# Kernel tuning notes

Hardware: AMD Instinct MI355X
Metric: run time of the kernel (lower is better)

The kernel has to match this reference:

```python
import math
import jax, jax.numpy as jnp
import numpy as np

Q = 24
N = 8
T_THETA = 1.0
R_S = 3.0
SIGMA_R = 1.0
RHO_MIN = 0.05
N_ORI = 4
TOL = 0.5


def _build_bank_7x7(n, tol=0.5, eps=1e-06):
    m = 3
    coords = np.arange(-m, m + 1, dtype=np.float32)
    u = coords.reshape(1, 1, 7)  # varies along width
    v = coords.reshape(1, 7, 1)  # varies along height
    Delta = math.pi / float(n)
    thetas = ((0.5 * Delta + np.arange(n, dtype=np.float32) * Delta) % math.pi).reshape(n, 1, 1)
    d = np.abs(-np.sin(thetas) * u + np.cos(thetas) * v)
    M = (d <= tol).astype(np.float32)
    M[:, m, m] = 1.0
    W = M[:, None, :, :]  # (n,1,7,7)
    denom = W.sum(axis=(1, 2, 3), keepdims=True) + eps
    return W / denom


def _bilinear_shift(Fm, dx, dy):
    """Shift-sample Fm (B,H,W) by (dx,dy) pixels, matching torch grid_sample
    (bilinear, zeros padding, align_corners=False) on linspace(-1,1) base grid."""
    B, H, W = Fm.shape
    xs = (jnp.arange(W, dtype=Fm.dtype) - dx) * (W / (W - 1)) - 0.5
    ys = (jnp.arange(H, dtype=Fm.dtype) - dy) * (H / (H - 1)) - 0.5

    def axis_parts(p, size):
        p0 = jnp.floor(p)
        f = p - p0
        i0 = p0.astype(jnp.int32)
        i1 = i0 + 1
        w0 = jnp.where((i0 >= 0) & (i0 < size), 1.0 - f, 0.0)
        w1 = jnp.where((i1 >= 0) & (i1 < size), f, 0.0)
        return jnp.clip(i0, 0, size - 1), jnp.clip(i1, 0, size - 1), w0, w1

    y0, y1, wy0, wy1 = axis_parts(ys, H)
    x0, x1, wx0, wx1 = axis_parts(xs, W)
    # separable bilinear: interpolate rows, then columns
    Fy = Fm[:, y0, :] * wy0[None, :, None] + Fm[:, y1, :] * wy1[None, :, None]
    return Fy[:, :, x0] * wx0[None, None, :] + Fy[:, :, x1] * wx1[None, None, :]


def _line_energy_theta(x):
    """x: (B,2,H,W) -> hat_theta (B,H,W) in [0, 2pi)."""
    Fm = jnp.sqrt(jnp.sum(x * x, axis=1))  # (B,H,W) L2 over channels
    t_n = jnp.arange(1, N + 1, dtype=x.dtype) / N * R_S
    w_n = jnp.exp(-t_n * t_n / (2.0 * SIGMA_R ** 2))
    w_n = w_n / w_n.sum()
    theta_q = 2.0 * jnp.pi * jnp.arange(Q, dtype=x.dtype) / Q
    cos_q, sin_q = jnp.cos(theta_q), jnp.sin(theta_q)

    def energy_one_angle(cs):
        c, s = cs
        # (N,B,H,W) samples along the ray, then radial weighted sum
        S = jax.vmap(lambda t: _bilinear_shift(Fm, t * c, t * s))(t_n)
        return jnp.tensordot(w_n, S, axes=1)  # (B,H,W)

    E = jax.lax.map(energy_one_angle, (cos_q, sin_q))  # (Q,B,H,W)
    pi_q = jax.nn.softmax(E / T_THETA, axis=0)
    sy = jnp.einsum('q,qbhw->bhw', sin_q, pi_q)
    cx = jnp.einsum('q,qbhw->bhw', cos_q, pi_q)
    hat = jnp.arctan2(sy, cx)
    return jnp.remainder(hat + 2.0 * jnp.pi, 2.0 * jnp.pi)


def setup_inputs() -> dict:
    key = jax.random.key(0)
    k1, = jax.random.split(key, 1)
    x = jax.random.normal(k1, (8, 2, 512, 512), dtype=jnp.float32)
    gain = jnp.ones((1,), dtype=jnp.float32)
    log_route_temp = jnp.asarray(math.log(0.08), dtype=jnp.float32)
    rho_scaled = (0.5 - RHO_MIN) / (1.0 - RHO_MIN)
    rho_logit = jnp.asarray(math.log(rho_scaled / (1.0 - rho_scaled)), dtype=jnp.float32)
    W_bank = jnp.asarray(_build_bank_7x7(N_ORI, tol=TOL))  # (4,1,7,7)
    Delta = math.pi / float(N_ORI)
    centers = (0.5 * Delta + np.arange(N_ORI, dtype=np.float32) * Delta).reshape(1, N_ORI, 1, 1)
    theta_centers = jnp.asarray(centers)
    return {"x": x, "gain": gain, "log_route_temp": log_route_temp,
            "rho_logit": rho_logit, "W_bank": W_bank, "theta_centers": theta_centers}


def reference(x, gain, log_route_temp, rho_logit, W_bank, theta_centers):
    hat_theta = _line_energy_theta(x)  # (B,H,W)
    # orientation bank conv: expand (n,1,7,7) -> (n,2,7,7), SAME padding (pad=3)
    w = jnp.broadcast_to(W_bank, (N_ORI, 2, 7, 7))
    y = jax.lax.conv_general_dilated(
        x, w, window_strides=(1, 1), padding=((3, 3), (3, 3)),
        dimension_numbers=('NCHW', 'OIHW', 'NCHW'))  # (B,n,H,W)
    # soft orientation routing
    theta = jnp.remainder(hat_theta, jnp.pi)[:, None, :, :]  # (B,1,H,W)
    delta = jnp.remainder(theta - theta_centers + 0.5 * jnp.pi, jnp.pi) - 0.5 * jnp.pi
    dist = jnp.abs(delta)  # (B,n,H,W)
    route_temp = jnp.clip(jnp.exp(log_route_temp), 0.001, 2.0)
    base = jax.nn.softmax(-dist / route_temp, axis=1)
    rho = jax.nn.sigmoid(rho_logit) * (1.0 - RHO_MIN) + RHO_MIN
    gamma = 1.0 / (rho + 1e-08)
    sharp = jnp.power(base + 1e-12, gamma)
    weights = sharp / (sharp.sum(axis=1, keepdims=True) + 1e-08)
    out = jnp.sum(y * weights, axis=1, keepdims=True)  # (B,1,H,W)
    return jnp.clip(gain, 0.001, None) * out
```

## Files before the change

kernel.cpp:

```cpp
#include <hip/hip_runtime.h>
#include <math.h>

#define TILE_W 64
#define TILE_H 4
#define HALO 4
#define TWX (TILE_W + 2*HALO)
#define TWY (TILE_H + 2*HALO)
#define NST (TWX*TWY)

#if __has_builtin(__builtin_amdgcn_fractf)
#define FRACTF(x) __builtin_amdgcn_fractf(x)
#else
#define FRACTF(x) ((x) - floorf(x))
#endif
#if __has_builtin(__builtin_amdgcn_exp2f)
#define EXP2F(x) __builtin_amdgcn_exp2f(x)
#else
#define EXP2F(x) exp2f(x)
#endif
#if __has_builtin(__builtin_amdgcn_logf)
#define LOG2F(x) __builtin_amdgcn_logf(x)
#else
#define LOG2F(x) log2f(x)
#endif

__global__ __launch_bounds__(64) void gp_setup(const float* __restrict__ gain,
                                               const float* __restrict__ lrt,
                                               const float* __restrict__ rlg,
                                               const float* __restrict__ Wb,
                                               float* __restrict__ tbl) {
  int t = threadIdx.x;
  __shared__ float wtmp[8];
  if (t < 8) {
    float tn = (float)(t + 1) * 0.375f;
    wtmp[t] = expf(-0.5f * tn * tn);
  }
  if (t < 24) {
    float th = (6.283185307179586f * (float)t) / 24.0f;
    float c = cosf(th), s = sinf(th);
    const float sc = (float)(512.0 / 511.0);
    tbl[t]      = c;
    tbl[24 + t] = s;
    tbl[48 + t] = c * sc;
    tbl[72 + t] = s * sc;
  }
  __syncthreads();
  if (t == 0) {
    const float L2E = 1.44269504088896340736f;
    float sum = 0.f;
    for (int n = 0; n < 8; ++n) sum += wtmp[n];
    for (int n = 0; n < 8; ++n) tbl[96 + n] = (wtmp[n] / sum) * L2E;
    float rt = expf(lrt[0]);
    rt = fminf(fmaxf(rt, 0.001f), 2.0f);
    float sg = 1.0f / (1.0f + expf(-rlg[0]));
    float rho = sg * 0.95f + 0.05f;
    tbl[104] = (1.0f / rt) * L2E;
    tbl[105] = 1.0f / (rho + 1e-8f);
    tbl[106] = fmaxf(gain[0], 0.001f);
    int* ti = (int*)tbl;
    int dense = 0;
    for (int o = 0; o < 4; ++o) {
      int cnt = 0;
      for (int k = 0; k < 49; ++k) {
        float w = Wb[o * 49 + k];
        if (w != 0.0f) {
          if (cnt < 8) {
            int kj = k / 7, ki = k - kj * 7;
            tbl[108 + o * 8 + cnt] = w;
            ti[140 + o * 8 + cnt] = kj * TWX + ki;
          }
          cnt++;
        }
      }
      if (cnt > 8) dense = 1;
      for (int c2 = cnt; c2 < 8; ++c2) { tbl[108 + o * 8 + c2] = 0.f; ti[140 + o * 8 + c2] = 0; }
    }
    ti[107] = dense;
  }
}

__global__ __launch_bounds__(256) void gp_main(const float* __restrict__ x,
                                               const float* __restrict__ Wb,
                                               const float* __restrict__ cen,
                                               const float* __restrict__ tbl,
                                               float* __restrict__ out) {
  __shared__ float  Fm[NST];
  __shared__ float  Sm[NST];
  __shared__ float4 Qd[NST];

  const int tx = threadIdx.x;
  const int ty = threadIdx.y;
  const int tid = ty * 64 + tx;
  const int bx0 = blockIdx.x * TILE_W - HALO;
  const int by0 = blockIdx.y * TILE_H - HALO;
  const int b = blockIdx.z;
  const float* __restrict__ x0p = x + (size_t)b * 2 * 512 * 512;
  const float* __restrict__ x1p = x0p + 512 * 512;

  #pragma unroll
  for (int it = 0; it < 4; ++it) {
    int idx = tid + it * 256;
    if (idx < NST) {
      int r = idx / TWX, c = idx - r * TWX;
      int gy = by0 + r, gx = bx0 + c;
      float a = 0.f, bv = 0.f;
      if ((unsigned)gx < 512u && (unsigned)gy < 512u) {
        size_t o = (size_t)gy * 512 + gx;
        a = x0p[o];
        bv = x1p[o];
      }
      Fm[idx] = sqrtf(a * a + bv * bv);
      Sm[idx] = a + bv;
    }
  }
  __syncthreads();
  #pragma unroll
  for (int it = 0; it < 4; ++it) {
    int idx = tid + it * 256;
    if (idx < NST) {
      int r = idx / TWX, c = idx - r * TWX;
      int r1 = (r < TWY - 1) ? r + 1 : r;
      int c1 = (c < TWX - 1) ? c + 1 : c;
      float v00 = Fm[r * TWX + c],  v01 = Fm[r * TWX + c1];
      float v10 = Fm[r1 * TWX + c], v11 = Fm[r1 * TWX + c1];
      Qd[idx] = make_float4(v00, v01 - v00, v10 - v00, (v11 - v10) - (v01 - v00));
    }
  }
  __syncthreads();

  const int gi = bx0 + HALO + tx;
  const int gj = by0 + HALO + ty;
  const float SC = (float)(512.0 / 511.0);
  const float axl = fmaf((float)gi, SC, -0.5f) - (float)bx0;
  const float ayl = fmaf((float)gj, SC, -0.5f) - (float)by0;

  float wn[8];
  #pragma unroll
  for (int n = 0; n < 8; ++n) wn[n] = tbl[96 + n];

  float SY = 0.f, CX = 0.f;
  for (int q = 0; q < 24; ++q) {
    const float csx = tbl[48 + q];
    const float ssy = tbl[72 + q];
    float e2 = 0.f;
    #pragma unroll
    for (int n = 0; n < 8; ++n) {
      const float tn = 0.375f * (float)(n + 1);
      float px = fmaf(-csx, tn, axl);
      float py = fmaf(-ssy, tn, ayl);
      int ix = (int)px;
      int iy = (int)py;
      float fx = FRACTF(px);
      float fy = FRACTF(py);
      float4 v = Qd[iy * TWX + ix];
      float fxy = fx * fy;
      float s = fmaf(fx, v.y, v.x);
      s = fmaf(fy, v.z, s);
      s = fmaf(fxy, v.w, s);
      e2 = fmaf(wn[n], s, e2);
    }
    float e = EXP2F(e2);
    SY = fmaf(e, tbl[24 + q], SY);
    CX = fmaf(e, tbl[q], CX);
  }

  const int* ti = (const int*)tbl;
  const int cbase = (ty + 1) * TWX + tx + 1;
  float a0 = 0.f, a1 = 0.f, a2 = 0.f, a3 = 0.f;
  if (ti[107] == 0) {
    #pragma unroll
    for (int t2 = 0; t2 < 8; ++t2) {
      a0 = fmaf(Sm[cbase + ti[140 + t2]],      tbl[108 + t2],      a0);
      a1 = fmaf(Sm[cbase + ti[148 + t2]],      tbl[116 + t2],      a1);
      a2 = fmaf(Sm[cbase + ti[156 + t2]],      tbl[124 + t2],      a2);
      a3 = fmaf(Sm[cbase + ti[164 + t2]],      tbl[132 + t2],      a3);
    }
  } else {
    #pragma unroll
    for (int kj = 0; kj < 7; ++kj) {
      #pragma unroll
      for (int ki = 0; ki < 7; ++ki) {
        float s = Sm[(ty + 1 + kj) * TWX + (tx + 1 + ki)];
        int k = kj * 7 + ki;
        a0 = fmaf(s, Wb[k], a0);
        a1 = fmaf(s, Wb[49 + k], a1);
        a2 = fmaf(s, Wb[98 + k], a2);
        a3 = fmaf(s, Wb[147 + k], a3);
      }
    }
  }

  const float TP  = 6.283185307179586f;
  const float PIF = 3.14159265358979323846f;
  const float HP  = 1.57079632679489661923f;
  float hat = atan2f(SY, CX);
  float r1 = hat + TP;
  r1 = (r1 >= TP) ? (r1 - TP) : r1;
  float theta = (r1 >= PIF) ? (r1 - PIF) : r1;

  const float irt2  = tbl[104];
  const float gamma = tbl[105];
  const float gainc = tbl[106];

  float dist[4];
  #pragma unroll
  for (int o = 0; o < 4; ++o) {
    float d = theta - cen[o] + HP;
    d -= (d >= PIF) ? PIF : 0.f;
    d += (d < 0.f) ? PIF : 0.f;
    dist[o] = fabsf(d - HP);
  }
  float mn = fminf(fminf(dist[0], dist[1]), fminf(dist[2], dist[3]));
  float m2 = mn * irt2;
  float eo[4], Z = 0.f;
  #pragma unroll
  for (int o = 0; o < 4; ++o) { eo[o] = EXP2F(fmaf(-irt2, dist[o], m2)); Z += eo[o]; }
  float invZ = 1.0f / Z;
  float sh[4], Zs = 0.f;
  #pragma unroll
  for (int o = 0; o < 4; ++o) {
    sh[o] = EXP2F(gamma * LOG2F(fmaf(eo[o], invZ, 1e-12f)));
    Zs += sh[o];
  }
  float wsi = 1.0f / (Zs + 1e-8f);
  float ov = (a0 * sh[0] + a1 * sh[1] + a2 * sh[2] + a3 * sh[3]) * wsi;

  out[((size_t)b * 512 + gj) * 512 + gi] = gainc * ov;
}

extern "C" void kernel_launch(void* const* d_in, const int* in_sizes, int n_in,
                              void* d_out, int out_size, void* d_ws, size_t ws_size,
                              hipStream_t stream) {
  const float* x    = (const float*)d_in[0];
  const float* gain = (const float*)d_in[1];
  const float* lrt  = (const float*)d_in[2];
  const float* rlg  = (const float*)d_in[3];
  const float* Wb   = (const float*)d_in[4];
  const float* cen  = (const float*)d_in[5];
  float* tbl = (float*)d_ws;

  gp_setup<<<1, 64, 0, stream>>>(gain, lrt, rlg, Wb, tbl);

  dim3 grid(512 / TILE_W, 512 / TILE_H, 8);
  dim3 blk(TILE_W, TILE_H);
  gp_main<<<grid, blk, 0, stream>>>(x, Wb, cen, tbl, (float*)d_out);
}
```

Before: 146.5 us.

## Precompute global bilinear quad image and split ray samples between LDS and global

Adds a pre-pass kernel that builds a padded global image of bilinear quad coefficients, so the main kernel loads its LDS tile directly instead of computing norms and differences per block. Odd ray samples (which reach beyond the tile halo) are fetched from the global quad image through the cache, while even samples use LDS. The main kernel also gets a swizzled block order and a specialised orientation convolution that uses shared horizontal and vertical sums when the bank matches the expected 7-tap line patterns. The cost is an extra kernel launch and a large workspace write and read of float4 data.

```diff
diff --git a/kernel.cpp b/kernel.cpp
--- a/kernel.cpp
+++ b/kernel.cpp
@@ -4,9 +4,11 @@
 #define TILE_W 64
 #define TILE_H 4
 #define HALO 4
-#define TWX (TILE_W + 2*HALO)
-#define TWY (TILE_H + 2*HALO)
+#define TWX 72
+#define TWY 12
 #define NST (TWX*TWY)
+#define QIW 528
+#define QIH 520
 
 #if __has_builtin(__builtin_amdgcn_fractf)
 #define FRACTF(x) __builtin_amdgcn_fractf(x)
@@ -39,10 +41,7 @@
     float th = (6.283185307179586f * (float)t) / 24.0f;
     float c = cosf(th), s = sinf(th);
     const float sc = (float)(512.0 / 511.0);
-    tbl[t]      = c;
-    tbl[24 + t] = s;
-    tbl[48 + t] = c * sc;
-    tbl[72 + t] = s * sc;
+    tbl[t] = c; tbl[24 + t] = s; tbl[48 + t] = c * sc; tbl[72 + t] = s * sc;
   }
   __syncthreads();
   if (t == 0) {
@@ -57,6 +56,7 @@
     tbl[104] = (1.0f / rt) * L2E;
     tbl[105] = 1.0f / (rho + 1e-8f);
     tbl[106] = fmaxf(gain[0], 0.001f);
+
     int* ti = (int*)tbl;
     int dense = 0;
     for (int o = 0; o < 4; ++o) {
@@ -76,18 +76,220 @@
       for (int c2 = cnt; c2 < 8; ++c2) { tbl[108 + o * 8 + c2] = 0.f; ti[140 + o * 8 + c2] = 0; }
     }
     ti[107] = dense;
-  }
-}
-
-__global__ __launch_bounds__(256) void gp_main(const float* __restrict__ x,
-                                               const float* __restrict__ Wb,
-                                               const float* __restrict__ cen,
-                                               const float* __restrict__ tbl,
-                                               float* __restrict__ out) {
+
+    const int K0[7] = {14,15,23,24,25,33,34};
+    const int K1[7] = {2,9,17,24,31,39,46};
+    const int K2[7] = {4,11,17,24,31,37,44};
+    const int K3[7] = {19,20,23,24,25,28,29};
+    const int* KK[4] = {K0,K1,K2,K3};
+    int ok = 1;
+    for (int o = 0; o < 4; ++o) {
+      float w0v = Wb[o * 49 + KK[o][0]];
+      if (w0v == 0.f) ok = 0;
+      unsigned long long mask = 0;
+      for (int t2 = 0; t2 < 7; ++t2) mask |= 1ull << KK[o][t2];
+      for (int k = 0; k < 49; ++k) {
+        float w = Wb[o * 49 + k];
+        int nz = (w != 0.f);
+        int want = (int)((mask >> k) & 1ull);
+        if (nz != want) ok = 0;
+        if (nz && w != w0v) ok = 0;
+      }
+      tbl[180 + o] = w0v;
+    }
+    ti[172] = ok;
+  }
+}
+
+__device__ inline float fmv(const float* __restrict__ x0p, const float* __restrict__ x1p,
+                            int Y, int X) {
+  if ((unsigned)X < 512u && (unsigned)Y < 512u) {
+    size_t o = (size_t)Y * 512 + X;
+    float a = x0p[o], b = x1p[o];
+    return sqrtf(a * a + b * b);
+  }
+  return 0.f;
+}
+
+__global__ __launch_bounds__(256) void gp_quad(const float* __restrict__ x,
+                                               float4* __restrict__ qimg) {
+  int xx = blockIdx.x * 64 + (threadIdx.x & 63);
+  int yy = blockIdx.y * 4 + (threadIdx.x >> 6);
+  int b = blockIdx.z;
+  if (xx >= QIH) return;
+  const float* x0p = x + (size_t)b * 2 * 512 * 512;
+  const float* x1p = x0p + 512 * 512;
+  int X = xx - 4, Y = yy - 4;
+  float f00 = fmv(x0p, x1p, Y, X);
+  float f01 = fmv(x0p, x1p, Y, X + 1);
+  float f10 = fmv(x0p, x1p, Y + 1, X);
+  float f11 = fmv(x0p, x1p, Y + 1, X + 1);
+  qimg[((size_t)b * QIH + yy) * QIW + xx] =
+      make_float4(f00, f01 - f00, f10 - f00, (f11 - f10) - (f01 - f00));
+}
+
+__global__ __launch_bounds__(256) void gp_main2(const float* __restrict__ x,
+                                                const float4* __restrict__ qimg,
+                                                const float* __restrict__ Wb,
+                                                const float* __restrict__ cen,
+                                                const float* __restrict__ tbl,
+                                                float* __restrict__ out) {
+  __shared__ float4 Qd[1024];
+  __shared__ float  Sm[NST];
+
+  const int tid = threadIdx.x;
+  const int tx = tid & 63, ty = tid >> 6;
+  int wg = blockIdx.x;
+  int swz = (wg & 7) * 1024 + (wg >> 3);
+  int bx = swz & 7;
+  int by = (swz >> 3) & 127;
+  int b  = swz >> 10;
+
+  const int bx0 = bx * 64 - HALO, by0 = by * 4 - HALO;
+  const float* __restrict__ x0p = x + (size_t)b * 2 * 512 * 512;
+  const float* __restrict__ x1p = x0p + 512 * 512;
+  const float4* __restrict__ qb = qimg + ((size_t)b * QIH + (by * 4)) * QIW + (bx * 64);
+
+  #pragma unroll
+  for (int it = 0; it < 4; ++it) {
+    int idx = tid + it * 256;
+    int i2 = (idx < NST) ? idx : (NST - 1);
+    int r = i2 / TWX, c = i2 - r * TWX;
+    Qd[idx] = qb[r * QIW + c];
+  }
+  #pragma unroll
+  for (int it = 0; it < 4; ++it) {
+    int idx = tid + it * 256;
+    if (idx < NST) {
+      int r = idx / TWX, c = idx - r * TWX;
+      int gy = by0 + r, gx = bx0 + c;
+      float a = 0.f, bv = 0.f;
+      if ((unsigned)gx < 512u && (unsigned)gy < 512u) {
+        size_t o = (size_t)gy * 512 + gx;
+        a = x0p[o]; bv = x1p[o];
+      }
+      Sm[idx] = a + bv;
+    }
+  }
+  __syncthreads();
+
+  const int gi = bx * 64 + tx;
+  const int gj = by * 4 + ty;
+  const float SC = (float)(512.0 / 511.0);
+  const float axl = fmaf((float)gi, SC, -0.5f) - (float)bx0;
+  const float ayl = fmaf((float)gj, SC, -0.5f) - (float)by0;
+
+  float wn[8];
+  #pragma unroll
+  for (int n = 0; n < 8; ++n) wn[n] = tbl[96 + n];
+
+  float SY = 0.f, CX = 0.f;
+  for (int q = 0; q < 24; ++q) {
+    const float csx = tbl[48 + q];
+    const float ssy = tbl[72 + q];
+    float4 vm[4]; float fxs[4], fys[4];
+    #pragma unroll
+    for (int h = 0; h < 4; ++h) {
+      float tn = 0.75f * (float)(h + 1);
+      float px = fmaf(-csx, tn, axl);
+      float py = fmaf(-ssy, tn, ayl);
+      int ix = (int)px, iy = (int)py;
+      fxs[h] = FRACTF(px); fys[h] = FRACTF(py);
+      vm[h] = qb[iy * QIW + ix];
+    }
+    float e2 = 0.f;
+    #pragma unroll
+    for (int n = 0; n < 8; ++n) {
+      float s;
+      if (n & 1) {
+        int h = n >> 1;
+        float4 v = vm[h];
+        float fx = fxs[h], fy = fys[h];
+        s = fmaf(fx * fy, v.w, fmaf(fy, v.z, fmaf(fx, v.y, v.x)));
+      } else {
+        float tn = 0.375f * (float)(n + 1);
+        float px = fmaf(-csx, tn, axl);
+        float py = fmaf(-ssy, tn, ayl);
+        int ix = (int)px, iy = (int)py;
+        float fx = FRACTF(px), fy = FRACTF(py);
+        float4 v = Qd[iy * TWX + ix];
+        s = fmaf(fx * fy, v.w, fmaf(fy, v.z, fmaf(fx, v.y, v.x)));
+      }
+      e2 = fmaf(wn[n], s, e2);
+    }
+    float e = EXP2F(e2);
+    SY = fmaf(e, tbl[24 + q], SY);
+    CX = fmaf(e, tbl[q], CX);
+  }
+
+  const int* ti = (const int*)tbl;
+  const int ccen = (ty + 4) * TWX + tx + 4;
+  float a0, a1, a2, a3;
+  if (ti[172]) {
+    float sCt = Sm[ccen];
+    float H3 = (Sm[ccen - 1] + sCt) + Sm[ccen + 1];
+    float V3 = (Sm[ccen - TWX] + sCt) + Sm[ccen + TWX];
+    a0 = tbl[180] * (H3 + ((Sm[ccen - 75] + Sm[ccen - 74]) + (Sm[ccen + 74] + Sm[ccen + 75])));
+    a1 = tbl[181] * (V3 + ((Sm[ccen - 217] + Sm[ccen - 145]) + (Sm[ccen + 145] + Sm[ccen + 217])));
+    a2 = tbl[182] * (V3 + ((Sm[ccen - 215] + Sm[ccen - 143]) + (Sm[ccen + 143] + Sm[ccen + 215])));
+    a3 = tbl[183] * (H3 + ((Sm[ccen - 70] + Sm[ccen - 69]) + (Sm[ccen + 69] + Sm[ccen + 70])));
+  } else {
+    a0 = a1 = a2 = a3 = 0.f;
+    for (int kj = 0; kj < 7; ++kj)
+      for (int ki = 0; ki < 7; ++ki) {
+        float s = Sm[(ty + 1 + kj) * TWX + (tx + 1 + ki)];
+        int k = kj * 7 + ki;
+        a0 = fmaf(s, Wb[k], a0); a1 = fmaf(s, Wb[49 + k], a1);
+        a2 = fmaf(s, Wb[98 + k], a2); a3 = fmaf(s, Wb[147 + k], a3);
+      }
+  }
+
+  const float TP  = 6.283185307179586f;
+  const float PIF = 3.14159265358979323846f;
+  const float HP  = 1.57079632679489661923f;
+  float hat = atan2f(SY, CX);
+  float r1 = hat + TP;
+  r1 = (r1 >= TP) ? (r1 - TP) : r1;
+  float theta = (r1 >= PIF) ? (r1 - PIF) : r1;
+
+  const float irt2  = tbl[104];
+  const float gamma = tbl[105];
+  const float gainc = tbl[106];
+
+  float dist[4];
+  #pragma unroll
+  for (int o = 0; o < 4; ++o) {
+    float d = theta - cen[o] + HP;
+    d -= (d >= PIF) ? PIF : 0.f;
+    d += (d < 0.f) ? PIF : 0.f;
+    dist[o] = fabsf(d - HP);
+  }
+  float mn = fminf(fminf(dist[0], dist[1]), fminf(dist[2], dist[3]));
+  float m2 = mn * irt2;
+  float eo[4], Z = 0.f;
+  #pragma unroll
+  for (int o = 0; o < 4; ++o) { eo[o] = EXP2F(fmaf(-irt2, dist[o], m2)); Z += eo[o]; }
+  float invZ = 1.0f / Z;
+  float sh[4], Zs = 0.f;
+  #pragma unroll
+  for (int o = 0; o < 4; ++o) {
+    sh[o] = EXP2F(gamma * LOG2F(fmaf(eo[o], invZ, 1e-12f)));
+    Zs += sh[o];
+  }
+  float wsi = 1.0f / (Zs + 1e-8f);
+  float ov = (a0 * sh[0] + a1 * sh[1] + a2 * sh[2] + a3 * sh[3]) * wsi;
+
+  out[((size_t)b * 512 + gj) * 512 + gi] = gainc * ov;
+}
+
+__global__ __launch_bounds__(256) void gp_main_fb(const float* __restrict__ x,
+                                                  const float* __restrict__ Wb,
+                                                  const float* __restrict__ cen,
+                                                  const float* __restrict__ tbl,
+                                                  float* __restrict__ out) {
   __shared__ float  Fm[NST];
   __shared__ float  Sm[NST];
   __shared__ float4 Qd[NST];
-
   const int tx = threadIdx.x;
   const int ty = threadIdx.y;
   const int tid = ty * 64 + tx;
@@ -96,7 +298,6 @@
   const int b = blockIdx.z;
   const float* __restrict__ x0p = x + (size_t)b * 2 * 512 * 512;
   const float* __restrict__ x1p = x0p + 512 * 512;
-
   #pragma unroll
   for (int it = 0; it < 4; ++it) {
     int idx = tid + it * 256;
@@ -106,8 +307,7 @@
       float a = 0.f, bv = 0.f;
       if ((unsigned)gx < 512u && (unsigned)gy < 512u) {
         size_t o = (size_t)gy * 512 + gx;
-        a = x0p[o];
-        bv = x1p[o];
+        a = x0p[o]; bv = x1p[o];
       }
       Fm[idx] = sqrtf(a * a + bv * bv);
       Sm[idx] = a + bv;
@@ -127,17 +327,14 @@
     }
   }
   __syncthreads();
-
   const int gi = bx0 + HALO + tx;
   const int gj = by0 + HALO + ty;
   const float SC = (float)(512.0 / 511.0);
   const float axl = fmaf((float)gi, SC, -0.5f) - (float)bx0;
   const float ayl = fmaf((float)gj, SC, -0.5f) - (float)by0;
-
   float wn[8];
   #pragma unroll
   for (int n = 0; n < 8; ++n) wn[n] = tbl[96 + n];
-
   float SY = 0.f, CX = 0.f;
   for (int q = 0; q < 24; ++q) {
     const float csx = tbl[48 + q];
@@ -148,48 +345,36 @@
       const float tn = 0.375f * (float)(n + 1);
       float px = fmaf(-csx, tn, axl);
       float py = fmaf(-ssy, tn, ayl);
-      int ix = (int)px;
-      int iy = (int)py;
-      float fx = FRACTF(px);
-      float fy = FRACTF(py);
+      int ix = (int)px, iy = (int)py;
+      float fx = FRACTF(px), fy = FRACTF(py);
       float4 v = Qd[iy * TWX + ix];
-      float fxy = fx * fy;
-      float s = fmaf(fx, v.y, v.x);
-      s = fmaf(fy, v.z, s);
-      s = fmaf(fxy, v.w, s);
+      float s = fmaf(fx * fy, v.w, fmaf(fy, v.z, fmaf(fx, v.y, v.x)));
       e2 = fmaf(wn[n], s, e2);
     }
     float e = EXP2F(e2);
     SY = fmaf(e, tbl[24 + q], SY);
     CX = fmaf(e, tbl[q], CX);
   }
-
   const int* ti = (const int*)tbl;
   const int cbase = (ty + 1) * TWX + tx + 1;
   float a0 = 0.f, a1 = 0.f, a2 = 0.f, a3 = 0.f;
   if (ti[107] == 0) {
     #pragma unroll
     for (int t2 = 0; t2 < 8; ++t2) {
-      a0 = fmaf(Sm[cbase + ti[140 + t2]],      tbl[108 + t2],      a0);
-      a1 = fmaf(Sm[cbase + ti[148 + t2]],      tbl[116 + t2],      a1);
-      a2 = fmaf(Sm[cbase + ti[156 + t2]],      tbl[124 + t2],      a2);
-      a3 = fmaf(Sm[cbase + ti[164 + t2]],      tbl[132 + t2],      a3);
+      a0 = fmaf(Sm[cbase + ti[140 + t2]], tbl[108 + t2], a0);
+      a1 = fmaf(Sm[cbase + ti[148 + t2]], tbl[116 + t2], a1);
+      a2 = fmaf(Sm[cbase + ti[156 + t2]], tbl[124 + t2], a2);
+      a3 = fmaf(Sm[cbase + ti[164 + t2]], tbl[132 + t2], a3);
     }
   } else {
-    #pragma unroll
-    for (int kj = 0; kj < 7; ++kj) {
-      #pragma unroll
+    for (int kj = 0; kj < 7; ++kj)
       for (int ki = 0; ki < 7; ++ki) {
         float s = Sm[(ty + 1 + kj) * TWX + (tx + 1 + ki)];
         int k = kj * 7 + ki;
-        a0 = fmaf(s, Wb[k], a0);
-        a1 = fmaf(s, Wb[49 + k], a1);
-        a2 = fmaf(s, Wb[98 + k], a2);
-        a3 = fmaf(s, Wb[147 + k], a3);
-      }
-    }
-  }
-
+        a0 = fmaf(s, Wb[k], a0); a1 = fmaf(s, Wb[49 + k], a1);
+        a2 = fmaf(s, Wb[98 + k], a2); a3 = fmaf(s, Wb[147 + k], a3);
+      }
+  }
   const float TP  = 6.283185307179586f;
   const float PIF = 3.14159265358979323846f;
   const float HP  = 1.57079632679489661923f;
@@ -197,11 +382,9 @@
   float r1 = hat + TP;
   r1 = (r1 >= TP) ? (r1 - TP) : r1;
   float theta = (r1 >= PIF) ? (r1 - PIF) : r1;
-
   const float irt2  = tbl[104];
   const float gamma = tbl[105];
   const float gainc = tbl[106];
-
   float dist[4];
   #pragma unroll
   for (int o = 0; o < 4; ++o) {
@@ -224,7 +407,6 @@
   }
   float wsi = 1.0f / (Zs + 1e-8f);
   float ov = (a0 * sh[0] + a1 * sh[1] + a2 * sh[2] + a3 * sh[3]) * wsi;
-
   out[((size_t)b * 512 + gj) * 512 + gi] = gainc * ov;
 }
 
@@ -241,7 +423,12 @@
 
   gp_setup<<<1, 64, 0, stream>>>(gain, lrt, rlg, Wb, tbl);
 
-  dim3 grid(512 / TILE_W, 512 / TILE_H, 8);
-  dim3 blk(TILE_W, TILE_H);
-  gp_main<<<grid, blk, 0, stream>>>(x, Wb, cen, tbl, (float*)d_out);
-}
+  size_t need = 4096 + (size_t)8 * QIH * QIW * sizeof(float4);
+  if (ws_size >= need) {
+    float4* qimg = (float4*)((char*)d_ws + 4096);
+    gp_quad<<<dim3((QIH + 63) / 64, QIH / 4, 8), dim3(256), 0, stream>>>(x, qimg);
+    gp_main2<<<dim3(8192), dim3(256), 0, stream>>>(x, qimg, Wb, cen, tbl, (float*)d_out);
+  } else {
+    gp_main_fb<<<dim3(8, 128, 8), dim3(64, 4), 0, stream>>>(x, Wb, cen, tbl, (float*)d_out);
+  }
+}
```

Measured after the change: 173.0 us. +18.1%, slower.
